# Kernel optimization log

Hardware: AMD Instinct MI355X
Metric: run time of the kernel (lower is better)

The kernel has to match this reference:

```python
import jax, jax.numpy as jnp
import numpy as np

# Dimensions
T = 1024      # tokens
D = 1024      # d_model
DFF = 1024    # expert intermediate dim
R = 64        # tucker rank (r_in == r_out)
G = 8         # n_group
E = 32        # experts_per_group
NEXP = G * E  # 256 routed experts
K = 8         # top-k


def setup_inputs() -> dict:
    key = jax.random.key(0)
    ks = jax.random.split(key, 12)
    s = 0.02
    return {
        "x": jax.random.normal(ks[0], (T, D), jnp.float32),
        "Wg": jax.random.normal(ks[1], (D, NEXP), jnp.float32) * s,
        "uin_gate": jax.random.normal(ks[2], (G, D, R), jnp.float32) * s,
        "core_gate": jax.random.normal(ks[3], (G, E, R, R), jnp.float32) * s,
        "uout_gate": jax.random.normal(ks[4], (G, R, DFF), jnp.float32) * s,
        "uin_up": jax.random.normal(ks[5], (G, D, R), jnp.float32) * s,
        "core_up": jax.random.normal(ks[6], (G, E, R, R), jnp.float32) * s,
        "uout_up": jax.random.normal(ks[7], (G, R, DFF), jnp.float32) * s,
        "uin_down": jax.random.normal(ks[8], (G, DFF, R), jnp.float32) * s,
        "core_down": jax.random.normal(ks[9], (G, E, R, R), jnp.float32) * s,
        "uout_down": jax.random.normal(ks[10], (G, R, D), jnp.float32) * s,
    }


def _moe_forward(x, Wg, uin_gate, core_gate, uout_gate,
                 uin_up, core_up, uout_up,
                 uin_down, core_down, uout_down):
    Tn, d = x.shape
    # Router: top-k over 256 experts, softmax over the k logits (fp32 as in torch)
    logits = x @ Wg                                   # [T, NEXP]
    w, sel = jax.lax.top_k(logits, K)                 # [T, K]
    w = jax.nn.softmax(w.astype(jnp.float32), axis=-1).astype(x.dtype)

    e = sel.reshape(-1)                               # [F] global expert id
    g = e // E                                        # [F] group id
    tok = jnp.repeat(jnp.arange(Tn), K)               # [F] source token id
    mask = (g[:, None] == jnp.arange(G)[None, :]).astype(x.dtype)  # [F, G]

    def gather_in(uin):
        # project tokens with every group's u_in once, then gather per pair
        pre = jnp.einsum('td,gdr->gtr', x, uin)       # [G, T, R]
        return pre[g, tok]                            # [F, R]

    def core_apply(xin, core):
        # per-pair Tucker core slice bmm: x.unsqueeze(1) @ core[rel_idx]
        slices = core.reshape(G * E, R, R)[e]         # [F, R, R] gather
        return jnp.einsum('fr,fro->fo', xin, slices)  # [F, R]

    def group_out(h, U):
        # per-pair group-specific projection: h[f] @ U[g_f]
        out = jnp.zeros((h.shape[0], U.shape[-1]), h.dtype)
        for gi in range(G):  # fixed small loop over 8 groups
            out = out + (h * mask[:, gi:gi + 1]) @ U[gi]
        return out

    gate_h = group_out(core_apply(gather_in(uin_gate), core_gate), uout_gate)  # [F, DFF]
    up_h = group_out(core_apply(gather_in(uin_up), core_up), uout_up)          # [F, DFF]
    act = jax.nn.silu(gate_h) * up_h                                           # SwiGLU
    xin_d = group_out(act, uin_down)                                           # [F, R]
    out_f = group_out(core_apply(xin_d, core_down), uout_down)                 # [F, D]
    out_f = out_f * w.reshape(-1)[:, None]
    # scatter-add expert outputs back to tokens
    return jax.ops.segment_sum(out_f, tok, num_segments=Tn)


def reference(x, Wg, uin_gate, core_gate, uout_gate,
              uin_up, core_up, uout_up,
              uin_down, core_down, uout_down):
    return _moe_forward(x, Wg, uin_gate, core_gate, uout_gate,
                        uin_up, core_up, uout_up,
                        uin_down, core_down, uout_down)
```

## Files before the change

### kernel.cpp

```cpp
#include <hip/hip_runtime.h>
#include <hip/hip_bf16.h>
#include <math.h>


#define T_ 1024
#define D_ 1024
#define DFF_ 1024
#define R_ 64
#define G_ 8
#define E_ 32
#define NEXP_ 256
#define K_ 8
#define F_ 8192
#define LKZ_ 4
#define PKZ_ 2
#define DKZ_ 4
#define LP_ 72

typedef short bf16x8 __attribute__((ext_vector_type(8)));
typedef float f32x4 __attribute__((ext_vector_type(4)));

__device__ __forceinline__ unsigned short f2bf(float f) {
  unsigned int u = __float_as_uint(f);
  u += 0x7fffu + ((u >> 16) & 1u);
  return (unsigned short)(u >> 16);
}

__device__ __forceinline__ void stage_tile(short* dst, const unsigned short* src,
                                           int gp, int tid) {
  for (int idx = tid; idx < 512; idx += 256) {
    int r = idx >> 3, c8 = (idx & 7) << 3;
    *(uint4*)&dst[r * LP_ + c8] = *(const uint4*)&src[(size_t)r * gp + c8];
  }
}

__device__ __forceinline__ void stage_tile_guard(short* dst, const unsigned short* src,
                                                 int gp, int rows_valid, int tid) {
  for (int idx = tid; idx < 512; idx += 256) {
    int r = idx >> 3, c8 = (idx & 7) << 3;
    uint4 v = make_uint4(0u, 0u, 0u, 0u);
    if (r < rows_valid) v = *(const uint4*)&src[(size_t)r * gp + c8];
    *(uint4*)&dst[r * LP_ + c8] = v;
  }
}

__device__ __forceinline__ void mma_strip(const short* As, const short* Bs,
                                          int ms, int lane, f32x4* acc) {
  int lm = lane & 15;
  int lk = (lane >> 4) << 3;
#pragma unroll
  for (int kc = 0; kc < 64; kc += 32) {
    bf16x8 a = *(const bf16x8*)&As[(ms + lm) * LP_ + kc + lk];
#pragma unroll
    for (int nt = 0; nt < 4; ++nt) {
      bf16x8 b = *(const bf16x8*)&Bs[(nt * 16 + lm) * LP_ + kc + lk];
      acc[nt] = __builtin_amdgcn_mfma_f32_16x16x32_bf16(a, b, acc[nt], 0, 0, 0);
    }
  }
}

__global__ __launch_bounds__(256) void k_cast_x(const float* __restrict__ x,
                                                unsigned short* __restrict__ xb) {
  int i = (blockIdx.x * 256 + threadIdx.x) * 4;
  float4 v = *(const float4*)&x[i];
  xb[i + 0] = f2bf(v.x);
  xb[i + 1] = f2bf(v.y);
  xb[i + 2] = f2bf(v.z);
  xb[i + 3] = f2bf(v.w);
}

__global__ __launch_bounds__(256) void k_castT(const float* __restrict__ s0, const float* __restrict__ s1,
                                               const float* __restrict__ s2, const float* __restrict__ s3,
                                               const float* __restrict__ s4, const float* __restrict__ s5,
                                               unsigned short* __restrict__ d0, unsigned short* __restrict__ d1,
                                               unsigned short* __restrict__ d2, unsigned short* __restrict__ d3,
                                               unsigned short* __restrict__ d4, unsigned short* __restrict__ d5) {
  __shared__ float ts[64][65];
  int id = blockIdx.z, g = blockIdx.y, tile = blockIdx.x;
  const float* src = id == 0 ? s0 : id == 1 ? s1 : id == 2 ? s2 : id == 3 ? s3 : id == 4 ? s4 : s5;
  unsigned short* dst = id == 0 ? d0 : id == 1 ? d1 : id == 2 ? d2 : id == 3 ? d3 : id == 4 ? d4 : d5;
  if (id < 3) {
    int r0 = tile * 64;
    for (int idx = threadIdx.x; idx < 4096; idx += 256) {
      int r = idx >> 6, c = idx & 63;
      ts[r][c] = src[((size_t)g * 1024 + r0 + r) * 64 + c];
    }
    __syncthreads();
    for (int idx = threadIdx.x; idx < 4096; idx += 256) {
      int c = idx >> 6, r = idx & 63;
      dst[((size_t)g * 64 + c) * 1024 + r0 + r] = f2bf(ts[r][c]);
    }
  } else {
    int c0 = tile * 64;
    for (int idx = threadIdx.x; idx < 4096; idx += 256) {
      int r = idx >> 6, c = idx & 63;
      ts[r][c] = src[((size_t)g * 64 + r) * 1024 + c0 + c];
    }
    __syncthreads();
    for (int idx = threadIdx.x; idx < 4096; idx += 256) {
      int c = idx >> 6, r = idx & 63;
      dst[((size_t)g * 1024 + c0 + c) * 64 + r] = f2bf(ts[r][c]);
    }
  }
}

__global__ __launch_bounds__(256) void k_logits(const float* __restrict__ x,
                                                const float* __restrict__ Wg,
                                                float* __restrict__ lp) {
  __shared__ float xs[4][64];
  int t0 = blockIdx.x * 4;
  int z = blockIdx.y;
  int e = threadIdx.x;
  float a0 = 0.f, a1 = 0.f, a2 = 0.f, a3 = 0.f;
  int dlo = z * (D_ / LKZ_), dhi = dlo + D_ / LKZ_;
  for (int dc = dlo; dc < dhi; dc += 64) {
    int tl = threadIdx.x >> 6, d = threadIdx.x & 63;
    xs[tl][d] = x[(t0 + tl) * D_ + dc + d];
    __syncthreads();
#pragma unroll 16
    for (int d2 = 0; d2 < 64; ++d2) {
      float wv = Wg[(size_t)(dc + d2) * NEXP_ + e];
      a0 = fmaf(xs[0][d2], wv, a0);
      a1 = fmaf(xs[1][d2], wv, a1);
      a2 = fmaf(xs[2][d2], wv, a2);
      a3 = fmaf(xs[3][d2], wv, a3);
    }
    __syncthreads();
  }
  size_t base = (size_t)z * T_ * NEXP_;
  lp[base + (size_t)(t0 + 0) * NEXP_ + e] = a0;
  lp[base + (size_t)(t0 + 1) * NEXP_ + e] = a1;
  lp[base + (size_t)(t0 + 2) * NEXP_ + e] = a2;
  lp[base + (size_t)(t0 + 3) * NEXP_ + e] = a3;
}

__global__ __launch_bounds__(256) void k_topk(const float* __restrict__ lp,
                                              int* __restrict__ sel,
                                              float* __restrict__ wsm,
                                              int* __restrict__ cnt) {
  int wave = threadIdx.x >> 6;
  int lane = threadIdx.x & 63;
  int t = blockIdx.x * 4 + wave;

  float v[4];
  int idx[4];
#pragma unroll
  for (int j = 0; j < 4; ++j) {
    idx[j] = lane + 64 * j;
    float s = 0.f;
#pragma unroll
    for (int z = 0; z < LKZ_; ++z)
      s += lp[(size_t)z * T_ * NEXP_ + (size_t)t * NEXP_ + idx[j]];
    v[j] = s;
  }

  float topv[K_];
  int topi[K_];
#pragma unroll
  for (int k = 0; k < K_; ++k) {
    float bv = v[0];
    int bi = idx[0];
#pragma unroll
    for (int j = 1; j < 4; ++j)
      if (v[j] > bv || (v[j] == bv && idx[j] < bi)) { bv = v[j]; bi = idx[j]; }
#pragma unroll
    for (int off = 32; off > 0; off >>= 1) {
      float ov = __shfl_xor(bv, off);
      int oi = __shfl_xor(bi, off);
      if (ov > bv || (ov == bv && oi < bi)) { bv = ov; bi = oi; }
    }
    topv[k] = bv;
    topi[k] = bi;
#pragma unroll
    for (int j = 0; j < 4; ++j)
      if (idx[j] == bi) v[j] = -INFINITY;
  }

  float m = topv[0];
  float ev[K_];
  float s = 0.f;
#pragma unroll
  for (int k = 0; k < K_; ++k) { ev[k] = expf(topv[k] - m); s += ev[k]; }
  float inv = 1.f / s;
  if (lane < K_) {
    sel[t * K_ + lane] = topi[lane];
    wsm[t * K_ + lane] = ev[lane] * inv;
    atomicAdd(&cnt[topi[lane]], 1);
  }
}

__global__ __launch_bounds__(256) void k_scan(const int* __restrict__ cnt,
                                              int* __restrict__ off) {
  __shared__ int s[NEXP_];
  int i = threadIdx.x;
  s[i] = cnt[i];
  __syncthreads();
  for (int d = 1; d < NEXP_; d <<= 1) {
    int v = (i >= d) ? s[i - d] : 0;
    __syncthreads();
    s[i] += v;
    __syncthreads();
  }
  off[i + 1] = s[i];
  if (i == 0) off[0] = 0;
}

__global__ __launch_bounds__(256) void k_scatter(const int* __restrict__ sel,
                                                 const float* __restrict__ wsm,
                                                 const int* __restrict__ off,
                                                 int* __restrict__ cur,
                                                 int* __restrict__ stok,
                                                 int* __restrict__ se,
                                                 float* __restrict__ sw,
                                                 int* __restrict__ ipos) {
  int f = blockIdx.x * 256 + threadIdx.x;
  int e = sel[f];
  int p = off[e] + atomicAdd(&cur[e], 1);
  stok[p] = f >> 3;
  se[p] = e;
  sw[p] = wsm[f];
  ipos[f] = p;
}

__global__ __launch_bounds__(256) void k_pre_mfma(const unsigned short* __restrict__ xb,
                                                  const unsigned short* __restrict__ uinT_g,
                                                  const unsigned short* __restrict__ uinT_u,
                                                  float* __restrict__ Pgp,
                                                  float* __restrict__ Pup) {
  int g = blockIdx.y;
  int gu = blockIdx.z >> 1, kz = blockIdx.z & 1;
  const unsigned short* U = gu ? uinT_u : uinT_g;
  float* P = gu ? Pup : Pgp;
  int t0 = blockIdx.x * 64;
  __shared__ short As[64 * LP_], Bs[64 * LP_];
  int tid = threadIdx.x, lane = tid & 63, ms = (tid >> 6) * 16;
  f32x4 acc[4] = {};
  int dlo = kz * (D_ / PKZ_);
  for (int dc = dlo; dc < dlo + D_ / PKZ_; dc += 64) {
    stage_tile(As, xb + (size_t)t0 * D_ + dc, D_, tid);
    stage_tile(Bs, U + (size_t)g * 64 * 1024 + dc, 1024, tid);
    __syncthreads();
    mma_strip(As, Bs, ms, lane, acc);
    __syncthreads();
  }
  int lm = lane & 15, lq = (lane >> 4) * 4;
#pragma unroll
  for (int nt = 0; nt < 4; ++nt)
#pragma unroll
    for (int r = 0; r < 4; ++r)
      P[((size_t)(kz * G_ + g) * T_ + t0 + ms + lq + r) * R_ + nt * 16 + lm] = acc[nt][r];
}

__global__ __launch_bounds__(256) void k_core_gu(const float* __restrict__ Pgp,
                                                 const float* __restrict__ Pup,
                                                 const float* __restrict__ core_g,
                                                 const float* __restrict__ core_u,
                                                 const int* __restrict__ stok,
                                                 const int* __restrict__ se,
                                                 unsigned short* __restrict__ xgb,
                                                 unsigned short* __restrict__ xub) {
  int pl = threadIdx.x >> 6;
  int o = threadIdx.x & 63;
  int p = blockIdx.x * 4 + pl;
  int e = se[p];
  int t = stok[p];
  int g = e >> 5;
  __shared__ float rg[4][64], ru[4][64];
  float sg = 0.f, su = 0.f;
#pragma unroll
  for (int kz = 0; kz < PKZ_; ++kz) {
    sg += Pgp[((size_t)(kz * G_ + g) * T_ + t) * R_ + o];
    su += Pup[((size_t)(kz * G_ + g) * T_ + t) * R_ + o];
  }
  rg[pl][o] = sg;
  ru[pl][o] = su;
  __syncthreads();
  const float* cg = core_g + (size_t)e * R_ * R_;
  const float* cu = core_u + (size_t)e * R_ * R_;
  float ag = 0.f, au = 0.f;
#pragma unroll 8
  for (int r = 0; r < R_; ++r) {
    ag = fmaf(rg[pl][r], cg[r * R_ + o], ag);
    au = fmaf(ru[pl][r], cu[r * R_ + o], au);
  }
  xgb[(size_t)p * R_ + o] = f2bf(ag);
  xub[(size_t)p * R_ + o] = f2bf(au);
}

__global__ __launch_bounds__(256) void k_act_mfma(const unsigned short* __restrict__ xgb,
                                                  const unsigned short* __restrict__ xub,
                                                  const unsigned short* __restrict__ uoutT_g,
                                                  const unsigned short* __restrict__ uoutT_u,
                                                  const int* __restrict__ off,
                                                  unsigned short* __restrict__ act) {
  int g = blockIdx.y;
  int p0 = off[g * E_];
  int pend = off[g * E_ + E_];
  int ntiles = (pend - p0 + 63) >> 6;
  int c0 = blockIdx.z * 64;
  __shared__ short Ag[64 * LP_], Au[64 * LP_], Bg[64 * LP_], Bu[64 * LP_];
  int tid = threadIdx.x, lane = tid & 63, ms = (tid >> 6) * 16;
  int lm = lane & 15, lq = (lane >> 4) * 4;
  for (int tile = blockIdx.x; tile < ntiles; tile += gridDim.x) {
    int pbase = p0 + tile * 64;
    int rv = pend - pbase; if (rv > 64) rv = 64;
    stage_tile_guard(Ag, xgb + (size_t)pbase * R_, R_, rv, tid);
    stage_tile_guard(Au, xub + (size_t)pbase * R_, R_, rv, tid);
    stage_tile(Bg, uoutT_g + ((size_t)g * DFF_ + c0) * R_, R_, tid);
    stage_tile(Bu, uoutT_u + ((size_t)g * DFF_ + c0) * R_, R_, tid);
    __syncthreads();
    f32x4 accg[4] = {}, accu[4] = {};
    mma_strip(Ag, Bg, ms, lane, accg);
    mma_strip(Au, Bu, ms, lane, accu);
#pragma unroll
    for (int nt = 0; nt < 4; ++nt)
#pragma unroll
      for (int r = 0; r < 4; ++r) {
        float gv = accg[nt][r];
        float a = gv / (1.f + expf(-gv)) * accu[nt][r];
        Ag[(ms + lq + r) * LP_ + nt * 16 + lm] = (short)f2bf(a);
      }
    __syncthreads();
    for (int idx = tid; idx < 512; idx += 256) {
      int r = idx >> 3, c8 = (idx & 7) << 3;
      if (r < rv)
        *(uint4*)&act[((size_t)(pbase + r)) * DFF_ + c0 + c8] = *(const uint4*)&Ag[r * LP_ + c8];
    }
    __syncthreads();
  }
}

__global__ __launch_bounds__(256) void k_down_mfma(const unsigned short* __restrict__ act,
                                                   const unsigned short* __restrict__ uinT_d,
                                                   const int* __restrict__ off,
                                                   float* __restrict__ xdp) {
  int g = blockIdx.y;
  int kz = blockIdx.z;
  int p0 = off[g * E_];
  int pend = off[g * E_ + E_];
  int ntiles = (pend - p0 + 63) >> 6;
  __shared__ short As[64 * LP_], Bs[64 * LP_];
  int tid = threadIdx.x, lane = tid & 63, ms = (tid >> 6) * 16;
  int lm = lane & 15, lq = (lane >> 4) * 4;
  int clo = kz * (DFF_ / DKZ_);
  for (int tile = blockIdx.x; tile < ntiles; tile += gridDim.x) {
    int pbase = p0 + tile * 64;
    int rv = pend - pbase; if (rv > 64) rv = 64;
    f32x4 acc[4] = {};
    for (int cc = clo; cc < clo + DFF_ / DKZ_; cc += 64) {
      stage_tile_guard(As, act + (size_t)pbase * DFF_ + cc, DFF_, rv, tid);
      stage_tile(Bs, uinT_d + (size_t)g * 64 * 1024 + cc, 1024, tid);
      __syncthreads();
      mma_strip(As, Bs, ms, lane, acc);
      __syncthreads();
    }
#pragma unroll
    for (int nt = 0; nt < 4; ++nt)
#pragma unroll
      for (int r = 0; r < 4; ++r) {
        int p = pbase + ms + lq + r;
        if (p < pend) xdp[((size_t)kz * F_ + p) * R_ + nt * 16 + lm] = acc[nt][r];
      }
  }
}

__global__ __launch_bounds__(256) void k_core_down(const float* __restrict__ xdp,
                                                   const float* __restrict__ core_d,
                                                   const int* __restrict__ se,
                                                   unsigned short* __restrict__ xd2b) {
  int pl = threadIdx.x >> 6;
  int o = threadIdx.x & 63;
  int p = blockIdx.x * 4 + pl;
  int e = se[p];
  __shared__ float rg[4][64];
  float s = 0.f;
#pragma unroll
  for (int kz = 0; kz < DKZ_; ++kz) s += xdp[((size_t)kz * F_ + p) * R_ + o];
  rg[pl][o] = s;
  __syncthreads();
  const float* cd = core_d + (size_t)e * R_ * R_;
  float a = 0.f;
#pragma unroll 8
  for (int r = 0; r < R_; ++r) a = fmaf(rg[pl][r], cd[r * R_ + o], a);
  xd2b[(size_t)p * R_ + o] = f2bf(a);
}

__global__ __launch_bounds__(256) void k_outf_mfma(const unsigned short* __restrict__ xd2b,
                                                   const unsigned short* __restrict__ uoutT_d,
                                                   const int* __restrict__ off,
                                                   const float* __restrict__ sw,
                                                   float* __restrict__ outf) {
  int g = blockIdx.y;
  int p0 = off[g * E_];
  int pend = off[g * E_ + E_];
  int ntiles = (pend - p0 + 63) >> 6;
  int c0 = blockIdx.z * 64;
  __shared__ short As[64 * LP_], Bs[64 * LP_];
  __shared__ float Os[64 * 68];
  int tid = threadIdx.x, lane = tid & 63, ms = (tid >> 6) * 16;
  int lm = lane & 15, lq = (lane >> 4) * 4;
  for (int tile = blockIdx.x; tile < ntiles; tile += gridDim.x) {
    int pbase = p0 + tile * 64;
    int rv = pend - pbase; if (rv > 64) rv = 64;
    stage_tile_guard(As, xd2b + (size_t)pbase * R_, R_, rv, tid);
    stage_tile(Bs, uoutT_d + ((size_t)g * D_ + c0) * R_, R_, tid);
    __syncthreads();
    f32x4 acc[4] = {};
    mma_strip(As, Bs, ms, lane, acc);
    float wv[4];
#pragma unroll
    for (int r = 0; r < 4; ++r) {
      int p = pbase + ms + lq + r;
      wv[r] = (p < pend) ? sw[p] : 0.f;
    }
#pragma unroll
    for (int nt = 0; nt < 4; ++nt)
#pragma unroll
      for (int r = 0; r < 4; ++r)
        Os[(ms + lq + r) * 68 + nt * 16 + lm] = acc[nt][r] * wv[r];
    __syncthreads();
    for (int idx = tid; idx < 1024; idx += 256) {
      int r = idx >> 4, c4 = (idx & 15) << 2;
      if (r < rv)
        *(float4*)&outf[(size_t)(pbase + r) * D_ + c0 + c4] = *(const float4*)&Os[r * 68 + c4];
    }
    __syncthreads();
  }
}

__global__ __launch_bounds__(256) void k_gather(const float* __restrict__ outf,
                                                const int* __restrict__ ipos,
                                                float* __restrict__ out) {
  int t = blockIdx.x;
  __shared__ int pos[K_];
  if (threadIdx.x < K_) pos[threadIdx.x] = ipos[t * K_ + threadIdx.x];
  __syncthreads();
  int c = threadIdx.x * 4;
  float4 s = make_float4(0.f, 0.f, 0.f, 0.f);
#pragma unroll
  for (int k = 0; k < K_; ++k) {
    float4 v = *(const float4*)(outf + (size_t)pos[k] * D_ + c);
    s.x += v.x; s.y += v.y; s.z += v.z; s.w += v.w;
  }
  *(float4*)(out + (size_t)t * D_ + c) = s;
}

extern "C" void kernel_launch(void* const* d_in, const int* in_sizes, int n_in,
                              void* d_out, int out_size, void* d_ws, size_t ws_size,
                              hipStream_t stream) {
  const float* x = (const float*)d_in[0];
  const float* Wg = (const float*)d_in[1];
  const float* uin_gate = (const float*)d_in[2];
  const float* core_gate = (const float*)d_in[3];
  const float* uout_gate = (const float*)d_in[4];
  const float* uin_up = (const float*)d_in[5];
  const float* core_up = (const float*)d_in[6];
  const float* uout_up = (const float*)d_in[7];
  const float* uin_down = (const float*)d_in[8];
  const float* core_down = (const float*)d_in[9];
  const float* uout_down = (const float*)d_in[10];
  float* out = (float*)d_out;

  char* ws = (char*)d_ws;
  size_t o = 0;
  auto alloc = [&](size_t bytes) { size_t r = o; o = (o + bytes + 255) & ~(size_t)255; return r; };
  size_t o_lp = alloc((size_t)LKZ_ * T_ * NEXP_ * 4);
  size_t o_sel = alloc(F_ * 4);
  size_t o_wsm = alloc(F_ * 4);
  size_t o_cnt = alloc(NEXP_ * 4);
  size_t o_cur = alloc(NEXP_ * 4);
  size_t o_off = alloc((NEXP_ + 1) * 4);
  size_t o_stok = alloc(F_ * 4);
  size_t o_se = alloc(F_ * 4);
  size_t o_sw = alloc(F_ * 4);
  size_t o_ipos = alloc(F_ * 4);
  size_t o_xb = alloc((size_t)T_ * D_ * 2);
  size_t o_uinT_g = alloc((size_t)G_ * 64 * 1024 * 2);
  size_t o_uinT_u = alloc((size_t)G_ * 64 * 1024 * 2);
  size_t o_uinT_d = alloc((size_t)G_ * 64 * 1024 * 2);
  size_t o_uoutT_g = alloc((size_t)G_ * 1024 * 64 * 2);
  size_t o_uoutT_u = alloc((size_t)G_ * 1024 * 64 * 2);
  size_t o_uoutT_d = alloc((size_t)G_ * 1024 * 64 * 2);
  size_t o_xgb = alloc((size_t)F_ * R_ * 2);
  size_t o_xub = alloc((size_t)F_ * R_ * 2);
  size_t o_xd2b = alloc((size_t)F_ * R_ * 2);
  size_t o_union = alloc((size_t)F_ * D_ * 4);
  size_t o_act = o_union;
  size_t o_xdp = o_union + (size_t)16 * 1024 * 1024;
  size_t o_pgp = o_union + (size_t)24 * 1024 * 1024;
  size_t o_pup = o_union + (size_t)28 * 1024 * 1024;
  (void)ws_size;

  float* lp = (float*)(ws + o_lp);
  int* sel = (int*)(ws + o_sel);
  float* wsm = (float*)(ws + o_wsm);
  int* cnt = (int*)(ws + o_cnt);
  int* cur = (int*)(ws + o_cur);
  int* off = (int*)(ws + o_off);
  int* stok = (int*)(ws + o_stok);
  int* se = (int*)(ws + o_se);
  float* sw = (float*)(ws + o_sw);
  int* ipos = (int*)(ws + o_ipos);
  unsigned short* xb = (unsigned short*)(ws + o_xb);
  unsigned short* uinT_g = (unsigned short*)(ws + o_uinT_g);
  unsigned short* uinT_u = (unsigned short*)(ws + o_uinT_u);
  unsigned short* uinT_d = (unsigned short*)(ws + o_uinT_d);
  unsigned short* uoutT_g = (unsigned short*)(ws + o_uoutT_g);
  unsigned short* uoutT_u = (unsigned short*)(ws + o_uoutT_u);
  unsigned short* uoutT_d = (unsigned short*)(ws + o_uoutT_d);
  unsigned short* xgb = (unsigned short*)(ws + o_xgb);
  unsigned short* xub = (unsigned short*)(ws + o_xub);
  unsigned short* xd2b = (unsigned short*)(ws + o_xd2b);
  unsigned short* act = (unsigned short*)(ws + o_act);
  float* xdp = (float*)(ws + o_xdp);
  float* pgp = (float*)(ws + o_pgp);
  float* pup = (float*)(ws + o_pup);
  float* outf = (float*)(ws + o_union);

  hipMemsetAsync(cnt, 0, NEXP_ * 4, stream);
  hipMemsetAsync(cur, 0, NEXP_ * 4, stream);

  k_cast_x<<<T_ * D_ / 1024, 256, 0, stream>>>(x, xb);
  k_castT<<<dim3(16, G_, 6), 256, 0, stream>>>(uin_gate, uin_up, uin_down,
                                               uout_gate, uout_up, uout_down,
                                               uinT_g, uinT_u, uinT_d,
                                               uoutT_g, uoutT_u, uoutT_d);
  k_logits<<<dim3(T_ / 4, LKZ_), 256, 0, stream>>>(x, Wg, lp);
  k_topk<<<T_ / 4, 256, 0, stream>>>(lp, sel, wsm, cnt);
  k_scan<<<1, 256, 0, stream>>>(cnt, off);
  k_scatter<<<F_ / 256, 256, 0, stream>>>(sel, wsm, off, cur, stok, se, sw, ipos);
  k_pre_mfma<<<dim3(T_ / 64, G_, 2 * PKZ_), 256, 0, stream>>>(xb, uinT_g, uinT_u, pgp, pup);
  k_core_gu<<<F_ / 4, 256, 0, stream>>>(pgp, pup, core_gate, core_up, stok, se, xgb, xub);
  k_act_mfma<<<dim3(16, G_, DFF_ / 64), 256, 0, stream>>>(xgb, xub, uoutT_g, uoutT_u, off, act);
  k_down_mfma<<<dim3(16, G_, DKZ_), 256, 0, stream>>>(act, uinT_d, off, xdp);
  k_core_down<<<F_ / 4, 256, 0, stream>>>(xdp, core_down, se, xd2b);
  k_outf_mfma<<<dim3(16, G_, D_ / 64), 256, 0, stream>>>(xd2b, uoutT_d, off, sw, outf);
  k_gather<<<T_, 256, 0, stream>>>(outf, ipos, out);
}
```

Baseline: 231.5 us.

## Fuse router, sort, SwiGLU+down projection and replace gather with atomic scatter

```diff
diff --git a/kernel.cpp b/kernel.cpp
--- a/kernel.cpp
+++ b/kernel.cpp
@@ -12,7 +12,6 @@
 #define NEXP_ 256
 #define K_ 8
 #define F_ 8192
-#define LKZ_ 4
 #define PKZ_ 2
 #define DKZ_ 4
 #define LP_ 72
@@ -59,24 +58,30 @@
   }
 }
 
-__global__ __launch_bounds__(256) void k_cast_x(const float* __restrict__ x,
-                                                unsigned short* __restrict__ xb) {
-  int i = (blockIdx.x * 256 + threadIdx.x) * 4;
-  float4 v = *(const float4*)&x[i];
-  xb[i + 0] = f2bf(v.x);
-  xb[i + 1] = f2bf(v.y);
-  xb[i + 2] = f2bf(v.z);
-  xb[i + 3] = f2bf(v.w);
-}
-
-__global__ __launch_bounds__(256) void k_castT(const float* __restrict__ s0, const float* __restrict__ s1,
-                                               const float* __restrict__ s2, const float* __restrict__ s3,
-                                               const float* __restrict__ s4, const float* __restrict__ s5,
-                                               unsigned short* __restrict__ d0, unsigned short* __restrict__ d1,
-                                               unsigned short* __restrict__ d2, unsigned short* __restrict__ d3,
-                                               unsigned short* __restrict__ d4, unsigned short* __restrict__ d5) {
+__global__ __launch_bounds__(256) void k_prep(const float* __restrict__ x,
+                                              const float* __restrict__ s0, const float* __restrict__ s1,
+                                              const float* __restrict__ s2, const float* __restrict__ s3,
+                                              const float* __restrict__ s4, const float* __restrict__ s5,
+                                              unsigned short* __restrict__ xb,
+                                              unsigned short* __restrict__ d0, unsigned short* __restrict__ d1,
+                                              unsigned short* __restrict__ d2, unsigned short* __restrict__ d3,
+                                              unsigned short* __restrict__ d4, unsigned short* __restrict__ d5,
+                                              int* __restrict__ cnt, int* __restrict__ cur) {
+  int id = blockIdx.z, g = blockIdx.y, tile = blockIdx.x;
+  if (id == 6) {
+    size_t base = ((size_t)g * 16 + tile) * 8192;
+    for (int i = threadIdx.x; i < 2048; i += 256) {
+      size_t idx = base + (size_t)i * 4;
+      float4 v = *(const float4*)&x[idx];
+      xb[idx + 0] = f2bf(v.x);
+      xb[idx + 1] = f2bf(v.y);
+      xb[idx + 2] = f2bf(v.z);
+      xb[idx + 3] = f2bf(v.w);
+    }
+    if (g == 0 && tile == 0) { cnt[threadIdx.x] = 0; cur[threadIdx.x] = 0; }
+    return;
+  }
   __shared__ float ts[64][65];
-  int id = blockIdx.z, g = blockIdx.y, tile = blockIdx.x;
   const float* src = id == 0 ? s0 : id == 1 ? s1 : id == 2 ? s2 : id == 3 ? s3 : id == 4 ? s4 : s5;
   unsigned short* dst = id == 0 ? d0 : id == 1 ? d1 : id == 2 ? d2 : id == 3 ? d3 : id == 4 ? d4 : d5;
   if (id < 3) {
@@ -104,56 +109,36 @@
   }
 }
 
-__global__ __launch_bounds__(256) void k_logits(const float* __restrict__ x,
+__global__ __launch_bounds__(256) void k_router(const float* __restrict__ x,
                                                 const float* __restrict__ Wg,
-                                                float* __restrict__ lp) {
+                                                int* __restrict__ sel,
+                                                float* __restrict__ wsm,
+                                                int* __restrict__ cnt) {
   __shared__ float xs[4][64];
   int t0 = blockIdx.x * 4;
-  int z = blockIdx.y;
-  int e = threadIdx.x;
-  float a0 = 0.f, a1 = 0.f, a2 = 0.f, a3 = 0.f;
-  int dlo = z * (D_ / LKZ_), dhi = dlo + D_ / LKZ_;
-  for (int dc = dlo; dc < dhi; dc += 64) {
-    int tl = threadIdx.x >> 6, d = threadIdx.x & 63;
-    xs[tl][d] = x[(t0 + tl) * D_ + dc + d];
-    __syncthreads();
-#pragma unroll 16
-    for (int d2 = 0; d2 < 64; ++d2) {
-      float wv = Wg[(size_t)(dc + d2) * NEXP_ + e];
-      a0 = fmaf(xs[0][d2], wv, a0);
-      a1 = fmaf(xs[1][d2], wv, a1);
-      a2 = fmaf(xs[2][d2], wv, a2);
-      a3 = fmaf(xs[3][d2], wv, a3);
-    }
-    __syncthreads();
-  }
-  size_t base = (size_t)z * T_ * NEXP_;
-  lp[base + (size_t)(t0 + 0) * NEXP_ + e] = a0;
-  lp[base + (size_t)(t0 + 1) * NEXP_ + e] = a1;
-  lp[base + (size_t)(t0 + 2) * NEXP_ + e] = a2;
-  lp[base + (size_t)(t0 + 3) * NEXP_ + e] = a3;
-}
-
-__global__ __launch_bounds__(256) void k_topk(const float* __restrict__ lp,
-                                              int* __restrict__ sel,
-                                              float* __restrict__ wsm,
-                                              int* __restrict__ cnt) {
   int wave = threadIdx.x >> 6;
   int lane = threadIdx.x & 63;
-  int t = blockIdx.x * 4 + wave;
-
+  int t = t0 + wave;
+  float a[4] = {0.f, 0.f, 0.f, 0.f};
+  for (int dc = 0; dc < D_; dc += 64) {
+    int tl = threadIdx.x >> 6, d = threadIdx.x & 63;
+    xs[tl][d] = x[(size_t)(t0 + tl) * D_ + dc + d];
+    __syncthreads();
+#pragma unroll 8
+    for (int d2 = 0; d2 < 64; ++d2) {
+      float4 w4 = *(const float4*)&Wg[(size_t)(dc + d2) * NEXP_ + lane * 4];
+      float xv = xs[wave][d2];
+      a[0] = fmaf(xv, w4.x, a[0]);
+      a[1] = fmaf(xv, w4.y, a[1]);
+      a[2] = fmaf(xv, w4.z, a[2]);
+      a[3] = fmaf(xv, w4.w, a[3]);
+    }
+    __syncthreads();
+  }
   float v[4];
   int idx[4];
 #pragma unroll
-  for (int j = 0; j < 4; ++j) {
-    idx[j] = lane + 64 * j;
-    float s = 0.f;
-#pragma unroll
-    for (int z = 0; z < LKZ_; ++z)
-      s += lp[(size_t)z * T_ * NEXP_ + (size_t)t * NEXP_ + idx[j]];
-    v[j] = s;
-  }
-
+  for (int j = 0; j < 4; ++j) { v[j] = a[j]; idx[j] = lane * 4 + j; }
   float topv[K_];
   int topi[K_];
 #pragma unroll
@@ -175,7 +160,6 @@
     for (int j = 0; j < 4; ++j)
       if (idx[j] == bi) v[j] = -INFINITY;
   }
-
   float m = topv[0];
   float ev[K_];
   float s = 0.f;
@@ -189,9 +173,16 @@
   }
 }
 
-__global__ __launch_bounds__(256) void k_scan(const int* __restrict__ cnt,
-                                              int* __restrict__ off) {
+__global__ __launch_bounds__(256) void k_sortscan(const int* __restrict__ cnt,
+                                                  const int* __restrict__ sel,
+                                                  const float* __restrict__ wsm,
+                                                  int* __restrict__ off,
+                                                  int* __restrict__ stok,
+                                                  int* __restrict__ se,
+                                                  float* __restrict__ sw) {
   __shared__ int s[NEXP_];
+  __shared__ int offl[NEXP_];
+  __shared__ int curl[NEXP_];
   int i = threadIdx.x;
   s[i] = cnt[i];
   __syncthreads();
@@ -201,25 +192,18 @@
     s[i] += v;
     __syncthreads();
   }
+  offl[i] = s[i] - cnt[i];
+  curl[i] = 0;
   off[i + 1] = s[i];
   if (i == 0) off[0] = 0;
-}
-
-__global__ __launch_bounds__(256) void k_scatter(const int* __restrict__ sel,
-                                                 const float* __restrict__ wsm,
-                                                 const int* __restrict__ off,
-                                                 int* __restrict__ cur,
-                                                 int* __restrict__ stok,
-                                                 int* __restrict__ se,
-                                                 float* __restrict__ sw,
-                                                 int* __restrict__ ipos) {
-  int f = blockIdx.x * 256 + threadIdx.x;
-  int e = sel[f];
-  int p = off[e] + atomicAdd(&cur[e], 1);
-  stok[p] = f >> 3;
-  se[p] = e;
-  sw[p] = wsm[f];
-  ipos[f] = p;
+  __syncthreads();
+  for (int f = i; f < F_; f += 256) {
+    int e = sel[f];
+    int p = offl[e] + atomicAdd(&curl[e], 1);
+    stok[p] = f >> 3;
+    se[p] = e;
+    sw[p] = wsm[f];
+  }
 }
 
 __global__ __launch_bounds__(256) void k_pre_mfma(const unsigned short* __restrict__ xb,
@@ -287,18 +271,21 @@
   xub[(size_t)p * R_ + o] = f2bf(au);
 }
 
-__global__ __launch_bounds__(256) void k_act_mfma(const unsigned short* __restrict__ xgb,
+__global__ __launch_bounds__(256) void k_fused_ad(const unsigned short* __restrict__ xgb,
                                                   const unsigned short* __restrict__ xub,
                                                   const unsigned short* __restrict__ uoutT_g,
                                                   const unsigned short* __restrict__ uoutT_u,
+                                                  const unsigned short* __restrict__ uinT_d,
                                                   const int* __restrict__ off,
-                                                  unsigned short* __restrict__ act) {
+                                                  float* __restrict__ xdp) {
   int g = blockIdx.y;
+  int kz = blockIdx.z;
   int p0 = off[g * E_];
   int pend = off[g * E_ + E_];
   int ntiles = (pend - p0 + 63) >> 6;
-  int c0 = blockIdx.z * 64;
-  __shared__ short Ag[64 * LP_], Au[64 * LP_], Bg[64 * LP_], Bu[64 * LP_];
+  __shared__ short Ag[64 * LP_], Au[64 * LP_];
+  __shared__ short Bg[64 * LP_], Bu[64 * LP_], Bd[64 * LP_];
+  __shared__ short Pt[64 * LP_];
   int tid = threadIdx.x, lane = tid & 63, ms = (tid >> 6) * 16;
   int lm = lane & 15, lq = (lane >> 4) * 4;
   for (int tile = blockIdx.x; tile < ntiles; tile += gridDim.x) {
@@ -306,52 +293,26 @@
     int rv = pend - pbase; if (rv > 64) rv = 64;
     stage_tile_guard(Ag, xgb + (size_t)pbase * R_, R_, rv, tid);
     stage_tile_guard(Au, xub + (size_t)pbase * R_, R_, rv, tid);
-    stage_tile(Bg, uoutT_g + ((size_t)g * DFF_ + c0) * R_, R_, tid);
-    stage_tile(Bu, uoutT_u + ((size_t)g * DFF_ + c0) * R_, R_, tid);
-    __syncthreads();
-    f32x4 accg[4] = {}, accu[4] = {};
-    mma_strip(Ag, Bg, ms, lane, accg);
-    mma_strip(Au, Bu, ms, lane, accu);
-#pragma unroll
-    for (int nt = 0; nt < 4; ++nt)
-#pragma unroll
-      for (int r = 0; r < 4; ++r) {
-        float gv = accg[nt][r];
-        float a = gv / (1.f + expf(-gv)) * accu[nt][r];
-        Ag[(ms + lq + r) * LP_ + nt * 16 + lm] = (short)f2bf(a);
-      }
-    __syncthreads();
-    for (int idx = tid; idx < 512; idx += 256) {
-      int r = idx >> 3, c8 = (idx & 7) << 3;
-      if (r < rv)
-        *(uint4*)&act[((size_t)(pbase + r)) * DFF_ + c0 + c8] = *(const uint4*)&Ag[r * LP_ + c8];
-    }
-    __syncthreads();
-  }
-}
-
-__global__ __launch_bounds__(256) void k_down_mfma(const unsigned short* __restrict__ act,
-                                                   const unsigned short* __restrict__ uinT_d,
-                                                   const int* __restrict__ off,
-                                                   float* __restrict__ xdp) {
-  int g = blockIdx.y;
-  int kz = blockIdx.z;
-  int p0 = off[g * E_];
-  int pend = off[g * E_ + E_];
-  int ntiles = (pend - p0 + 63) >> 6;
-  __shared__ short As[64 * LP_], Bs[64 * LP_];
-  int tid = threadIdx.x, lane = tid & 63, ms = (tid >> 6) * 16;
-  int lm = lane & 15, lq = (lane >> 4) * 4;
-  int clo = kz * (DFF_ / DKZ_);
-  for (int tile = blockIdx.x; tile < ntiles; tile += gridDim.x) {
-    int pbase = p0 + tile * 64;
-    int rv = pend - pbase; if (rv > 64) rv = 64;
-    f32x4 acc[4] = {};
-    for (int cc = clo; cc < clo + DFF_ / DKZ_; cc += 64) {
-      stage_tile_guard(As, act + (size_t)pbase * DFF_ + cc, DFF_, rv, tid);
-      stage_tile(Bs, uinT_d + (size_t)g * 64 * 1024 + cc, 1024, tid);
+    f32x4 accd[4] = {};
+#pragma unroll
+    for (int c4 = 0; c4 < 4; ++c4) {
+      int cc = kz * (DFF_ / DKZ_) + c4 * 64;
+      stage_tile(Bg, uoutT_g + ((size_t)g * DFF_ + cc) * R_, R_, tid);
+      stage_tile(Bu, uoutT_u + ((size_t)g * DFF_ + cc) * R_, R_, tid);
+      stage_tile(Bd, uinT_d + (size_t)g * 64 * 1024 + cc, 1024, tid);
       __syncthreads();
-      mma_strip(As, Bs, ms, lane, acc);
+      f32x4 accg[4] = {}, accu[4] = {};
+      mma_strip(Ag, Bg, ms, lane, accg);
+      mma_strip(Au, Bu, ms, lane, accu);
+#pragma unroll
+      for (int nt = 0; nt < 4; ++nt)
+#pragma unroll
+        for (int r = 0; r < 4; ++r) {
+          float gv = accg[nt][r];
+          float av = gv / (1.f + expf(-gv)) * accu[nt][r];
+          Pt[(ms + lq + r) * LP_ + nt * 16 + lm] = (short)f2bf(av);
+        }
+      mma_strip(Pt, Bd, ms, lane, accd);
       __syncthreads();
     }
 #pragma unroll
@@ -359,8 +320,9 @@
 #pragma unroll
       for (int r = 0; r < 4; ++r) {
         int p = pbase + ms + lq + r;
-        if (p < pend) xdp[((size_t)kz * F_ + p) * R_ + nt * 16 + lm] = acc[nt][r];
+        if (p < pend) xdp[((size_t)kz * F_ + p) * R_ + nt * 16 + lm] = accd[nt][r];
       }
+    __syncthreads();
   }
 }
 
@@ -385,18 +347,18 @@
   xd2b[(size_t)p * R_ + o] = f2bf(a);
 }
 
-__global__ __launch_bounds__(256) void k_outf_mfma(const unsigned short* __restrict__ xd2b,
-                                                   const unsigned short* __restrict__ uoutT_d,
-                                                   const int* __restrict__ off,
-                                                   const float* __restrict__ sw,
-                                                   float* __restrict__ outf) {
+__global__ __launch_bounds__(256) void k_outf_atomic(const unsigned short* __restrict__ xd2b,
+                                                     const unsigned short* __restrict__ uoutT_d,
+                                                     const int* __restrict__ off,
+                                                     const float* __restrict__ sw,
+                                                     const int* __restrict__ stok,
+                                                     float* __restrict__ out) {
   int g = blockIdx.y;
   int p0 = off[g * E_];
   int pend = off[g * E_ + E_];
   int ntiles = (pend - p0 + 63) >> 6;
   int c0 = blockIdx.z * 64;
   __shared__ short As[64 * LP_], Bs[64 * LP_];
-  __shared__ float Os[64 * 68];
   int tid = threadIdx.x, lane = tid & 63, ms = (tid >> 6) * 16;
   int lm = lane & 15, lq = (lane >> 4) * 4;
   for (int tile = blockIdx.x; tile < ntiles; tile += gridDim.x) {
@@ -407,42 +369,19 @@
     __syncthreads();
     f32x4 acc[4] = {};
     mma_strip(As, Bs, ms, lane, acc);
-    float wv[4];
 #pragma unroll
     for (int r = 0; r < 4; ++r) {
       int p = pbase + ms + lq + r;
-      wv[r] = (p < pend) ? sw[p] : 0.f;
-    }
-#pragma unroll
-    for (int nt = 0; nt < 4; ++nt)
-#pragma unroll
-      for (int r = 0; r < 4; ++r)
-        Os[(ms + lq + r) * 68 + nt * 16 + lm] = acc[nt][r] * wv[r];
-    __syncthreads();
-    for (int idx = tid; idx < 1024; idx += 256) {
-      int r = idx >> 4, c4 = (idx & 15) << 2;
-      if (r < rv)
-        *(float4*)&outf[(size_t)(pbase + r) * D_ + c0 + c4] = *(const float4*)&Os[r * 68 + c4];
-    }
-    __syncthreads();
-  }
-}
-
-__global__ __launch_bounds__(256) void k_gather(const float* __restrict__ outf,
-                                                const int* __restrict__ ipos,
-                                                float* __restrict__ out) {
-  int t = blockIdx.x;
-  __shared__ int pos[K_];
-  if (threadIdx.x < K_) pos[threadIdx.x] = ipos[t * K_ + threadIdx.x];
-  __syncthreads();
-  int c = threadIdx.x * 4;
-  float4 s = make_float4(0.f, 0.f, 0.f, 0.f);
-#pragma unroll
-  for (int k = 0; k < K_; ++k) {
-    float4 v = *(const float4*)(outf + (size_t)pos[k] * D_ + c);
-    s.x += v.x; s.y += v.y; s.z += v.z; s.w += v.w;
-  }
-  *(float4*)(out + (size_t)t * D_ + c) = s;
+      if (p < pend) {
+        float wv = sw[p];
+        int t = stok[p];
+#pragma unroll
+        for (int nt = 0; nt < 4; ++nt)
+          atomicAdd(&out[(size_t)t * D_ + c0 + nt * 16 + lm], acc[nt][r] * wv);
+      }
+    }
+    __syncthreads();
+  }
 }
 
 extern "C" void kernel_launch(void* const* d_in, const int* in_sizes, int n_in,
@@ -464,7 +403,6 @@
   char* ws = (char*)d_ws;
   size_t o = 0;
   auto alloc = [&](size_t bytes) { size_t r = o; o = (o + bytes + 255) & ~(size_t)255; return r; };
-  size_t o_lp = alloc((size_t)LKZ_ * T_ * NEXP_ * 4);
   size_t o_sel = alloc(F_ * 4);
   size_t o_wsm = alloc(F_ * 4);
   size_t o_cnt = alloc(NEXP_ * 4);
@@ -473,7 +411,6 @@
   size_t o_stok = alloc(F_ * 4);
   size_t o_se = alloc(F_ * 4);
   size_t o_sw = alloc(F_ * 4);
-  size_t o_ipos = alloc(F_ * 4);
   size_t o_xb = alloc((size_t)T_ * D_ * 2);
   size_t o_uinT_g = alloc((size_t)G_ * 64 * 1024 * 2);
   size_t o_uinT_u = alloc((size_t)G_ * 64 * 1024 * 2);
@@ -484,14 +421,11 @@
   size_t o_xgb = alloc((size_t)F_ * R_ * 2);
   size_t o_xub = alloc((size_t)F_ * R_ * 2);
   size_t o_xd2b = alloc((size_t)F_ * R_ * 2);
-  size_t o_union = alloc((size_t)F_ * D_ * 4);
-  size_t o_act = o_union;
-  size_t o_xdp = o_union + (size_t)16 * 1024 * 1024;
-  size_t o_pgp = o_union + (size_t)24 * 1024 * 1024;
-  size_t o_pup = o_union + (size_t)28 * 1024 * 1024;
+  size_t o_pgp = alloc((size_t)PKZ_ * G_ * T_ * R_ * 4);
+  size_t o_pup = alloc((size_t)PKZ_ * G_ * T_ * R_ * 4);
+  size_t o_xdp = alloc((size_t)DKZ_ * F_ * R_ * 4);
   (void)ws_size;
 
-  float* lp = (float*)(ws + o_lp);
   int* sel = (int*)(ws + o_sel);
   float* wsm = (float*)(ws + o_wsm);
   int* cnt = (int*)(ws + o_cnt);
@@ -500,7 +434,6 @@
   int* stok = (int*)(ws + o_stok);
   int* se = (int*)(ws + o_se);
   float* sw = (float*)(ws + o_sw);
-  int* ipos = (int*)(ws + o_ipos);
   unsigned short* xb = (unsigned short*)(ws + o_xb);
   unsigned short* uinT_g = (unsigned short*)(ws + o_uinT_g);
   unsigned short* uinT_u = (unsigned short*)(ws + o_uinT_u);
@@ -511,29 +444,21 @@
   unsigned short* xgb = (unsigned short*)(ws + o_xgb);
   unsigned short* xub = (unsigned short*)(ws + o_xub);
   unsigned short* xd2b = (unsigned short*)(ws + o_xd2b);
-  unsigned short* act = (unsigned short*)(ws + o_act);
-  float* xdp = (float*)(ws + o_xdp);
   float* pgp = (float*)(ws + o_pgp);
   float* pup = (float*)(ws + o_pup);
-  float* outf = (float*)(ws + o_union);
-
-  hipMemsetAsync(cnt, 0, NEXP_ * 4, stream);
-  hipMemsetAsync(cur, 0, NEXP_ * 4, stream);
-
-  k_cast_x<<<T_ * D_ / 1024, 256, 0, stream>>>(x, xb);
-  k_castT<<<dim3(16, G_, 6), 256, 0, stream>>>(uin_gate, uin_up, uin_down,
-                                               uout_gate, uout_up, uout_down,
-                                               uinT_g, uinT_u, uinT_d,
-                                               uoutT_g, uoutT_u, uoutT_d);
-  k_logits<<<dim3(T_ / 4, LKZ_), 256, 0, stream>>>(x, Wg, lp);
-  k_topk<<<T_ / 4, 256, 0, stream>>>(lp, sel, wsm, cnt);
-  k_scan<<<1, 256, 0, stream>>>(cnt, off);
-  k_scatter<<<F_ / 256, 256, 0, stream>>>(sel, wsm, off, cur, stok, se, sw, ipos);
+  float* xdp = (float*)(ws + o_xdp);
+
+  hipMemsetAsync(out, 0, (size_t)T_ * D_ * 4, stream);
+
+  k_prep<<<dim3(16, G_, 7), 256, 0, stream>>>(x, uin_gate, uin_up, uin_down,
+                                              uout_gate, uout_up, uout_down, xb,
+                                              uinT_g, uinT_u, uinT_d,
+                                              uoutT_g, uoutT_u, uoutT_d, cnt, cur);
+  k_router<<<T_ / 4, 256, 0, stream>>>(x, Wg, sel, wsm, cnt);
+  k_sortscan<<<1, 256, 0, stream>>>(cnt, sel, wsm, off, stok, se, sw);
   k_pre_mfma<<<dim3(T_ / 64, G_, 2 * PKZ_), 256, 0, stream>>>(xb, uinT_g, uinT_u, pgp, pup);
   k_core_gu<<<F_ / 4, 256, 0, stream>>>(pgp, pup, core_gate, core_up, stok, se, xgb, xub);
-  k_act_mfma<<<dim3(16, G_, DFF_ / 64), 256, 0, stream>>>(xgb, xub, uoutT_g, uoutT_u, off, act);
-  k_down_mfma<<<dim3(16, G_, DKZ_), 256, 0, stream>>>(act, uinT_d, off, xdp);
+  k_fused_ad<<<dim3(16, G_, DKZ_), 256, 0, stream>>>(xgb, xub, uoutT_g, uoutT_u, uinT_d, off, xdp);
   k_core_down<<<F_ / 4, 256, 0, stream>>>(xdp, core_down, se, xd2b);
-  k_outf_mfma<<<dim3(16, G_, D_ / 64), 256, 0, stream>>>(xd2b, uoutT_d, off, sw, outf);
-  k_gather<<<T_, 256, 0, stream>>>(outf, ipos, out);
-}
+  k_outf_atomic<<<dim3(16, G_, D_ / 64), 256, 0, stream>>>(xd2b, uoutT_d, off, sw, stok, out);
+}
```

After: 279.1 us. +20.6%, slower.
